# Kernel optimization log

Hardware: AMD Instinct MI355X
Metric: run time of the kernel (lower is better)

The kernel has to match this reference:

```python
import jax, jax.numpy as jnp
import numpy as np

B, T, C = 4, 2048, 1024
HEAD = 64  # n_embd // n_heads


def setup_inputs() -> dict:
    key = jax.random.key(0)
    kx, kk, kq, kv = jax.random.split(key, 4)
    x = jax.random.normal(kx, (B, T, C), dtype=jnp.float32)
    # nn.Linear(n_embd, head_size, bias=False) weights have shape [head_size, n_embd]
    s = 1.0 / np.sqrt(C)
    Wk = jax.random.normal(kk, (HEAD, C), dtype=jnp.float32) * s
    Wq = jax.random.normal(kq, (HEAD, C), dtype=jnp.float32) * s
    Wv = jax.random.normal(kv, (HEAD, C), dtype=jnp.float32) * s
    return {"x": x, "Wk": Wk, "Wq": Wq, "Wv": Wv}


def reference(x, Wk, Wq, Wv):
    Bx, Tx, Cx = x.shape
    k = jnp.einsum("btc,hc->bth", x, Wk)  # [B,T,HEAD]
    q = jnp.einsum("btc,hc->bth", x, Wq)
    v = jnp.einsum("btc,hc->bth", x, Wv)
    # NOTE: original scales by C**-0.5 (C = n_embd), not head_size**-0.5
    scale = Cx ** (-0.5)
    wei = jnp.einsum("bth,bsh->bts", q, k) * scale  # [B,T,T]
    causal = jnp.tril(jnp.ones((Tx, Tx), dtype=bool))
    wei = jnp.where(causal, wei, -jnp.inf)
    wei = jax.nn.softmax(wei, axis=-1)
    # dropout p=0.0 (eval) -> identity
    out = jnp.einsum("bts,bsh->bth", wei, v)  # [B,T,HEAD]
    return out
```

## Files before the change

### kernel.cpp

```cpp
#include <hip/hip_runtime.h>
#include <math.h>

#define Tn 2048
#define Cn 1024
#define Hn 64

using u16 = unsigned short;
typedef float f32x4 __attribute__((ext_vector_type(4)));
typedef __bf16 bf16x8 __attribute__((ext_vector_type(8)));
typedef u16 u16x8 __attribute__((ext_vector_type(8)));
typedef u16 u16x4 __attribute__((ext_vector_type(4)));

__device__ __forceinline__ u16 f2bf(float f) {
    return __builtin_bit_cast(u16, static_cast<__bf16>(f));
}

#define SWI(r, c) ((r) * 64 + ((c) ^ (((r) & 7) << 3)))

#define LDS3(p) ((__attribute__((address_space(3))) void*)(p))
#define GLB1(p) ((const __attribute__((address_space(1))) void*)(p))

__global__ __launch_bounds__(256) void wpack_kernel(
    const float* __restrict__ Wk, const float* __restrict__ Wq,
    const float* __restrict__ Wv, u16* __restrict__ wp)
{
    int slot = blockIdx.x * 256 + threadIdx.x;
    int n16  = slot >> 11;
    int rem  = slot & 2047;
    int kc   = rem >> 6;
    int lane = rem & 63;
    int l15 = lane & 15, lg = lane >> 4;
    int col = n16 * 16 + l15;
    const float* __restrict__ Wm = (col < 64) ? Wk : (col < 128) ? Wq : Wv;
    float sc = (col >= 64 && col < 128) ? 0.03125f : 1.0f;
    const float* src = &Wm[(size_t)(col & 63) * Cn + kc * 32 + lg * 8];
    float4 lo = *reinterpret_cast<const float4*>(src);
    float4 hi = *reinterpret_cast<const float4*>(src + 4);
    u16x8 o;
    o[0] = f2bf(lo.x * sc); o[1] = f2bf(lo.y * sc);
    o[2] = f2bf(lo.z * sc); o[3] = f2bf(lo.w * sc);
    o[4] = f2bf(hi.x * sc); o[5] = f2bf(hi.y * sc);
    o[6] = f2bf(hi.z * sc); o[7] = f2bf(hi.w * sc);
    *reinterpret_cast<u16x8*>(&wp[(size_t)slot * 8]) = o;
}

__global__ __launch_bounds__(512) void qkv_proj(
    const float* __restrict__ x, const u16* __restrict__ wp,
    u16* __restrict__ kb, u16* __restrict__ qb, u16* __restrict__ vb)
{
    __shared__ float xs[2][32 * 68];

    const int tid  = threadIdx.x;
    const int lane = tid & 63;
    const int w    = tid >> 6;
    const int rg   = w & 1;
    const int cg   = w >> 1;
    const int l15  = lane & 15;
    const int lg   = lane >> 4;

    const int row0 = blockIdx.x * 32;
    const int sr   = tid >> 4;
    const int scc  = (tid & 15) << 2;

    f32x4 acc[3];
#pragma unroll
    for (int nt = 0; nt < 3; ++nt)
#pragma unroll
        for (int r = 0; r < 4; ++r) acc[nt][r] = 0.f;

    const float* __restrict__ xsrc = &x[(size_t)(row0 + sr) * Cn + scc];

    float4 g = *reinterpret_cast<const float4*>(xsrc);
    *reinterpret_cast<float4*>(&xs[0][sr * 68 + scc]) = g;
    __syncthreads();

    for (int ks = 0; ks < 16; ++ks) {
        const int cur = ks & 1;
        if (ks < 15)
            g = *reinterpret_cast<const float4*>(xsrc + (ks + 1) * 64);
#pragma unroll
        for (int kc2 = 0; kc2 < 2; ++kc2) {
            const float* ap = &xs[cur][(rg * 16 + l15) * 68 + kc2 * 32 + (lg << 3)];
            f32x4 a0 = *reinterpret_cast<const f32x4*>(ap);
            f32x4 a1 = *reinterpret_cast<const f32x4*>(ap + 4);
            bf16x8 a;
            a[0] = (__bf16)a0[0]; a[1] = (__bf16)a0[1];
            a[2] = (__bf16)a0[2]; a[3] = (__bf16)a0[3];
            a[4] = (__bf16)a1[0]; a[5] = (__bf16)a1[1];
            a[6] = (__bf16)a1[2]; a[7] = (__bf16)a1[3];
            const int kcg = ks * 2 + kc2;
#pragma unroll
            for (int nt = 0; nt < 3; ++nt) {
                const int n16 = cg * 3 + nt;
                bf16x8 bfr = *reinterpret_cast<const bf16x8*>(
                    &wp[(size_t)((n16 * 32 + kcg) * 64 + lane) * 8]);
                acc[nt] = __builtin_amdgcn_mfma_f32_16x16x32_bf16(a, bfr, acc[nt], 0, 0, 0);
            }
        }
        if (ks < 15)
            *reinterpret_cast<float4*>(&xs[cur ^ 1][sr * 68 + scc]) = g;
        __syncthreads();
    }

#pragma unroll
    for (int nt = 0; nt < 3; ++nt) {
        const int n16  = cg * 3 + nt;
        const int col0 = n16 * 16;
        const int mat  = col0 >> 6;
        u16* __restrict__ ob = (mat == 0) ? kb : (mat == 1) ? qb : vb;
        const int h = (col0 & 63) + l15;
#pragma unroll
        for (int reg = 0; reg < 4; ++reg) {
            const int grow = row0 + rg * 16 + (lg << 2) + reg;
            ob[(size_t)grow * Hn + h] = f2bf(acc[nt][reg]);
        }
    }
}

__global__ __launch_bounds__(256) void attn(
    const u16* __restrict__ qb, const u16* __restrict__ kb,
    const u16* __restrict__ vb, float* __restrict__ Opart,
    float* __restrict__ mlb)
{
    __shared__ u16 Ks[4][64 * 64];
    __shared__ u16 VTs[4][64 * 64];
    __shared__ u16 Pl[4][16 * 72];

    const int tid  = threadIdx.x;
    const int lane = tid & 63;
    const int w    = tid >> 6;
    const int g    = w >> 1;
    const int p    = w & 1;
    const int l15  = lane & 15;
    const int lg   = lane >> 4;

    const int bid = blockIdx.x;
    const int b = bid / 288;
    const int r = bid % 288;
    int gq = (int)((sqrtf((float)r + 1.0f) - 1.0f) * 0.5f);
    while (4 * (gq + 1) * (gq + 2) <= r) ++gq;
    while (4 * gq * (gq + 1) > r) --gq;
    const int rr = r - 4 * gq * (gq + 1);
    const int qt = gq * 8 + rr / (gq + 1);
    const int c  = rr % (gq + 1);
    const int c4 = c * 4;

    const int t0  = qt * 32;
    const int wr0 = t0 + g * 16;
    const int nkt = ((t0 + 31) >> 6) + 1;
    int ntt = nkt - c4; if (ntt > 4) ntt = 4;
    const size_t kvbase = (size_t)b * Tn * Hn;

    bf16x8 qf[2];
    {
        const u16* qrow = qb + ((size_t)(b * Tn + wr0 + l15)) * Hn;
        qf[0] = *reinterpret_cast<const bf16x8*>(&qrow[(lg << 3)]);
        qf[1] = *reinterpret_cast<const bf16x8*>(&qrow[32 + (lg << 3)]);
    }

    if (w < ntt) {
        const int kt = c4 + w;
        const u16* __restrict__ ksrc = kb + kvbase + (size_t)kt * 64 * Hn;
        const u16* __restrict__ vsrc = vb + kvbase + (size_t)(kt * 64 + lane) * Hn;
#pragma unroll
        for (int i = 0; i < 8; ++i) {
            const int rw = i * 8 + (lane >> 3);
            const int co = (((lane & 7) ^ (rw & 7)) << 3);
            __builtin_amdgcn_global_load_lds(
                GLB1(ksrc + rw * Hn + co), LDS3(&Ks[w][i * 512]), 16, 0, 0);
        }
        u16x8 vr[8];
#pragma unroll
        for (int i = 0; i < 8; ++i)
            vr[i] = *reinterpret_cast<const u16x8*>(&vsrc[i * 8]);
#pragma unroll
        for (int i = 0; i < 8; ++i)
#pragma unroll
            for (int j = 0; j < 8; ++j)
                VTs[w][SWI(i * 8 + j, lane)] = vr[i][j];
    }
    __syncthreads();

    f32x4 o[4];
    float m[4], ls[4];
#pragma unroll
    for (int nt = 0; nt < 4; ++nt)
#pragma unroll
        for (int rg2 = 0; rg2 < 4; ++rg2) o[nt][rg2] = 0.f;
#pragma unroll
    for (int rg2 = 0; rg2 < 4; ++rg2) { m[rg2] = -INFINITY; ls[rg2] = 0.f; }

#pragma unroll
    for (int s = 0; s < 2; ++s) {
        const int tt = 2 * s + p;
        const int mykt = c4 + tt;
        if (mykt < nkt) {
            f32x4 sf[4];
#pragma unroll
            for (int nt = 0; nt < 4; ++nt)
#pragma unroll
                for (int rg2 = 0; rg2 < 4; ++rg2) sf[nt][rg2] = 0.f;
            __builtin_amdgcn_s_setprio(1);
#pragma unroll
            for (int kc = 0; kc < 2; ++kc) {
#pragma unroll
                for (int nt = 0; nt < 4; ++nt) {
                    bf16x8 kf = *reinterpret_cast<const bf16x8*>(
                        &Ks[tt][SWI(nt * 16 + l15, kc * 32 + (lg << 3))]);
                    sf[nt] = __builtin_amdgcn_mfma_f32_16x16x32_bf16(qf[kc], kf, sf[nt], 0, 0, 0);
                }
            }
            __builtin_amdgcn_s_setprio(0);
            if (mykt * 64 + 63 > wr0) {
#pragma unroll
                for (int nt = 0; nt < 4; ++nt) {
                    int kg = mykt * 64 + nt * 16 + l15;
#pragma unroll
                    for (int reg = 0; reg < 4; ++reg) {
                        int tq = wr0 + (lg << 2) + reg;
                        if (kg > tq) sf[nt][reg] = -INFINITY;
                    }
                }
            }
            float tm[4];
            bool defok = true;
#pragma unroll
            for (int reg = 0; reg < 4; ++reg) {
                float t = fmaxf(fmaxf(sf[0][reg], sf[1][reg]),
                                fmaxf(sf[2][reg], sf[3][reg]));
#pragma unroll
                for (int off = 1; off < 16; off <<= 1)
                    t = fmaxf(t, __shfl_xor(t, off, 64));
                tm[reg] = t;
                defok = defok && (t <= m[reg] + 8.f);
            }
            if (!__all(defok ? 1 : 0)) {
#pragma unroll
                for (int reg = 0; reg < 4; ++reg) {
                    float nm = fmaxf(m[reg], tm[reg]);
                    float al = __expf(m[reg] - nm);
                    ls[reg] *= al;
#pragma unroll
                    for (int nt = 0; nt < 4; ++nt) o[nt][reg] *= al;
                    m[reg] = nm;
                }
            }
            float pv[4][4];
#pragma unroll
            for (int reg = 0; reg < 4; ++reg) {
                float rs = 0.f;
#pragma unroll
                for (int nt = 0; nt < 4; ++nt) {
                    pv[nt][reg] = __expf(sf[nt][reg] - m[reg]);
                    rs += pv[nt][reg];
                }
#pragma unroll
                for (int off = 1; off < 16; off <<= 1)
                    rs += __shfl_xor(rs, off, 64);
                ls[reg] += rs;
            }
#pragma unroll
            for (int nt = 0; nt < 4; ++nt)
#pragma unroll
                for (int reg = 0; reg < 4; ++reg)
                    Pl[w][((lg << 2) + reg) * 72 + nt * 16 + l15] = f2bf(pv[nt][reg]);
#pragma unroll
            for (int kc = 0; kc < 2; ++kc) {
                bf16x8 pa = *reinterpret_cast<const bf16x8*>(
                    &Pl[w][l15 * 72 + kc * 32 + (lg << 3)]);
                __builtin_amdgcn_s_setprio(1);
#pragma unroll
                for (int nt = 0; nt < 4; ++nt) {
                    bf16x8 vf = *reinterpret_cast<const bf16x8*>(
                        &VTs[tt][SWI(nt * 16 + l15, kc * 32 + (lg << 3))]);
                    o[nt] = __builtin_amdgcn_mfma_f32_16x16x32_bf16(pa, vf, o[nt], 0, 0, 0);
                }
                __builtin_amdgcn_s_setprio(0);
            }
        }
    }

    __syncthreads();
    float* slab = reinterpret_cast<float*>(&Ks[0][0]);
    float* sb = slab + g * (24 * 64);
    if (p == 1) {
#pragma unroll
        for (int nt = 0; nt < 4; ++nt)
#pragma unroll
            for (int reg = 0; reg < 4; ++reg)
                sb[(nt * 4 + reg) * 64 + lane] = o[nt][reg];
#pragma unroll
        for (int reg = 0; reg < 4; ++reg) {
            sb[(16 + reg) * 64 + lane] = m[reg];
            sb[(20 + reg) * 64 + lane] = ls[reg];
        }
    }
    __syncthreads();
    if (p == 0) {
        const size_t pidx = (size_t)(b * 64 + qt) * 8 + c;
        float* __restrict__ ob = Opart + pidx * 2048;
#pragma unroll
        for (int reg = 0; reg < 4; ++reg) {
            float mB = sb[(16 + reg) * 64 + lane];
            float lB = sb[(20 + reg) * 64 + lane];
            float ms = fmaxf(m[reg], mB);
            float aA = __expf(m[reg] - ms);
            float aB = __expf(mB - ms);
            int row32 = g * 16 + (lg << 2) + reg;
            if (l15 == 0) {
                float* mlp = mlb + pidx * 64 + row32 * 2;
                mlp[0] = ms;
                mlp[1] = aA * ls[reg] + aB * lB;
            }
#pragma unroll
            for (int nt = 0; nt < 4; ++nt)
                ob[row32 * 64 + nt * 16 + l15] =
                    aA * o[nt][reg] + aB * sb[(nt * 4 + reg) * 64 + lane];
        }
    }
}

__global__ __launch_bounds__(256) void attn_merge(
    const float* __restrict__ Opart, const float* __restrict__ mlb,
    float* __restrict__ out)
{
    const int bid = blockIdx.x;
    const int b = bid >> 6, qt = bid & 63;
    const int nch = (qt >> 3) + 1;
    const int t = threadIdx.x;
    const int row = t >> 3, d0 = (t & 7) << 3;
    const size_t pbase = (size_t)(b * 64 + qt) * 8;

    float mc[8], lc[8];
#pragma unroll
    for (int cc = 0; cc < 8; ++cc) {
        if (cc < nch) {
            const float* mlp = mlb + (pbase + cc) * 64 + row * 2;
            mc[cc] = mlp[0];
            lc[cc] = mlp[1];
        } else { mc[cc] = -INFINITY; lc[cc] = 0.f; }
    }
    float mfin = mc[0];
#pragma unroll
    for (int cc = 1; cc < 8; ++cc) mfin = fmaxf(mfin, mc[cc]);

    float wgt[8], l = 0.f;
#pragma unroll
    for (int cc = 0; cc < 8; ++cc) {
        wgt[cc] = (cc < nch) ? __expf(mc[cc] - mfin) : 0.f;
        l += lc[cc] * wgt[cc];
    }

    f32x4 O0 = {0.f, 0.f, 0.f, 0.f}, O1 = {0.f, 0.f, 0.f, 0.f};
#pragma unroll
    for (int cc = 0; cc < 8; ++cc) {
        if (cc < nch) {
            const float* op = Opart + (pbase + cc) * 2048 + row * 64 + d0;
            f32x4 c0 = *reinterpret_cast<const f32x4*>(op);
            f32x4 c1 = *reinterpret_cast<const f32x4*>(op + 4);
            O0 += c0 * wgt[cc];
            O1 += c1 * wgt[cc];
        }
    }
    float inv = 1.f / l;
    float* orow = out + ((size_t)(b * Tn + qt * 32 + row)) * Hn + d0;
    *reinterpret_cast<f32x4*>(orow)     = O0 * inv;
    *reinterpret_cast<f32x4*>(orow + 4) = O1 * inv;
}

extern "C" void kernel_launch(void* const* d_in, const int* in_sizes, int n_in,
                              void* d_out, int out_size, void* d_ws, size_t ws_size,
                              hipStream_t stream) {
    const float* x  = (const float*)d_in[0];
    const float* Wk = (const float*)d_in[1];
    const float* Wq = (const float*)d_in[2];
    const float* Wv = (const float*)d_in[3];
    float* out = (float*)d_out;

    const size_t rows = (size_t)4 * Tn;
    u16* kbuf = (u16*)d_ws;
    u16* qbuf = kbuf + rows * Hn;
    u16* vbuf = qbuf + rows * Hn;
    u16* wpk  = vbuf + rows * Hn;
    float* Opart = (float*)(wpk + 196608);
    float* mlb   = Opart + (size_t)4 * 64 * 8 * 2048;

    wpack_kernel<<<96, 256, 0, stream>>>(Wk, Wq, Wv, wpk);
    qkv_proj<<<256, 512, 0, stream>>>(x, wpk, kbuf, qbuf, vbuf);
    attn<<<1152, 256, 0, stream>>>(qbuf, kbuf, vbuf, Opart, mlb);
    attn_merge<<<256, 256, 0, stream>>>(Opart, mlb, out);
}
```

Measured before the change: 52.55 us.

## Stage K/V tiles two at a time with padded LDS instead of all four

Each block used to load up to four K/V tiles into LDS at once, with K going directly global-to-LDS and XOR swizzling. Now the block loads two tiles per step cooperatively across all threads, into padded (stride 72) buffers, and synchronises after each step. This halves the K/V LDS footprint, which could let more blocks sit on each CU. In exchange it gives up the async direct-to-LDS path, adds extra barriers, and serialises load and compute between steps.

```diff
diff --git a/kernel.cpp b/kernel.cpp
--- a/kernel.cpp
+++ b/kernel.cpp
@@ -14,11 +14,6 @@
 __device__ __forceinline__ u16 f2bf(float f) {
     return __builtin_bit_cast(u16, static_cast<__bf16>(f));
 }
-
-#define SWI(r, c) ((r) * 64 + ((c) ^ (((r) & 7) << 3)))
-
-#define LDS3(p) ((__attribute__((address_space(3))) void*)(p))
-#define GLB1(p) ((const __attribute__((address_space(1))) void*)(p))
 
 __global__ __launch_bounds__(256) void wpack_kernel(
     const float* __restrict__ Wk, const float* __restrict__ Wq,
@@ -122,8 +117,8 @@
     const u16* __restrict__ vb, float* __restrict__ Opart,
     float* __restrict__ mlb)
 {
-    __shared__ u16 Ks[4][64 * 64];
-    __shared__ u16 VTs[4][64 * 64];
+    __shared__ u16 Ks[2][64 * 72];
+    __shared__ u16 VTs[2][64 * 72];
     __shared__ u16 Pl[4][16 * 72];
 
     const int tid  = threadIdx.x;
@@ -143,12 +138,10 @@
     const int rr = r - 4 * gq * (gq + 1);
     const int qt = gq * 8 + rr / (gq + 1);
     const int c  = rr % (gq + 1);
-    const int c4 = c * 4;
 
     const int t0  = qt * 32;
     const int wr0 = t0 + g * 16;
     const int nkt = ((t0 + 31) >> 6) + 1;
-    int ntt = nkt - c4; if (ntt > 4) ntt = 4;
     const size_t kvbase = (size_t)b * Tn * Hn;
 
     bf16x8 qf[2];
@@ -158,29 +151,6 @@
         qf[1] = *reinterpret_cast<const bf16x8*>(&qrow[32 + (lg << 3)]);
     }
 
-    if (w < ntt) {
-        const int kt = c4 + w;
-        const u16* __restrict__ ksrc = kb + kvbase + (size_t)kt * 64 * Hn;
-        const u16* __restrict__ vsrc = vb + kvbase + (size_t)(kt * 64 + lane) * Hn;
-#pragma unroll
-        for (int i = 0; i < 8; ++i) {
-            const int rw = i * 8 + (lane >> 3);
-            const int co = (((lane & 7) ^ (rw & 7)) << 3);
-            __builtin_amdgcn_global_load_lds(
-                GLB1(ksrc + rw * Hn + co), LDS3(&Ks[w][i * 512]), 16, 0, 0);
-        }
-        u16x8 vr[8];
-#pragma unroll
-        for (int i = 0; i < 8; ++i)
-            vr[i] = *reinterpret_cast<const u16x8*>(&vsrc[i * 8]);
-#pragma unroll
-        for (int i = 0; i < 8; ++i)
-#pragma unroll
-            for (int j = 0; j < 8; ++j)
-                VTs[w][SWI(i * 8 + j, lane)] = vr[i][j];
-    }
-    __syncthreads();
-
     f32x4 o[4];
     float m[4], ls[4];
 #pragma unroll
@@ -190,10 +160,45 @@
 #pragma unroll
     for (int rg2 = 0; rg2 < 4; ++rg2) { m[rg2] = -INFINITY; ls[rg2] = 0.f; }
 
-#pragma unroll
     for (int s = 0; s < 2; ++s) {
-        const int tt = 2 * s + p;
-        const int mykt = c4 + tt;
+        const int kt0 = c * 4 + 2 * s, kt1 = kt0 + 1;
+        if (kt0 < nkt) {
+#pragma unroll
+            for (int i = 0; i < 2; ++i) {
+                int cc = tid + 256 * i;
+                int rr2 = cc >> 3, c8 = (cc & 7) << 3;
+                *reinterpret_cast<u16x8*>(&Ks[0][rr2 * 72 + c8]) =
+                    *reinterpret_cast<const u16x8*>(&kb[kvbase + (size_t)(kt0 * 64 + rr2) * Hn + c8]);
+            }
+#pragma unroll
+            for (int i = 0; i < 2; ++i) {
+                int cc = tid + 256 * i;
+                int k = cc & 63, d0 = (cc >> 6) << 3;
+                u16x8 v = *reinterpret_cast<const u16x8*>(&vb[kvbase + (size_t)(kt0 * 64 + k) * Hn + d0]);
+#pragma unroll
+                for (int j = 0; j < 8; ++j) VTs[0][(d0 + j) * 72 + k] = v[j];
+            }
+        }
+        if (kt1 < nkt) {
+#pragma unroll
+            for (int i = 0; i < 2; ++i) {
+                int cc = tid + 256 * i;
+                int rr2 = cc >> 3, c8 = (cc & 7) << 3;
+                *reinterpret_cast<u16x8*>(&Ks[1][rr2 * 72 + c8]) =
+                    *reinterpret_cast<const u16x8*>(&kb[kvbase + (size_t)(kt1 * 64 + rr2) * Hn + c8]);
+            }
+#pragma unroll
+            for (int i = 0; i < 2; ++i) {
+                int cc = tid + 256 * i;
+                int k = cc & 63, d0 = (cc >> 6) << 3;
+                u16x8 v = *reinterpret_cast<const u16x8*>(&vb[kvbase + (size_t)(kt1 * 64 + k) * Hn + d0]);
+#pragma unroll
+                for (int j = 0; j < 8; ++j) VTs[1][(d0 + j) * 72 + k] = v[j];
+            }
+        }
+        __syncthreads();
+
+        const int mykt = kt0 + p;
         if (mykt < nkt) {
             f32x4 sf[4];
 #pragma unroll
@@ -206,7 +211,7 @@
 #pragma unroll
                 for (int nt = 0; nt < 4; ++nt) {
                     bf16x8 kf = *reinterpret_cast<const bf16x8*>(
-                        &Ks[tt][SWI(nt * 16 + l15, kc * 32 + (lg << 3))]);
+                        &Ks[p][(nt * 16 + l15) * 72 + kc * 32 + (lg << 3)]);
                     sf[nt] = __builtin_amdgcn_mfma_f32_16x16x32_bf16(qf[kc], kf, sf[nt], 0, 0, 0);
                 }
             }
@@ -272,15 +277,15 @@
 #pragma unroll
                 for (int nt = 0; nt < 4; ++nt) {
                     bf16x8 vf = *reinterpret_cast<const bf16x8*>(
-                        &VTs[tt][SWI(nt * 16 + l15, kc * 32 + (lg << 3))]);
+                        &VTs[p][(nt * 16 + l15) * 72 + kc * 32 + (lg << 3)]);
                     o[nt] = __builtin_amdgcn_mfma_f32_16x16x32_bf16(pa, vf, o[nt], 0, 0, 0);
                 }
                 __builtin_amdgcn_s_setprio(0);
             }
         }
-    }
-
-    __syncthreads();
+        __syncthreads();
+    }
+
     float* slab = reinterpret_cast<float*>(&Ks[0][0]);
     float* sb = slab + g * (24 * 64);
     if (p == 1) {
```

Result: faster. 49.22 us (-6.3%).
